# Performance work log

Hardware: AMD Instinct MI355X
Metric: run time of the kernel (lower is better)

The kernel has to match this reference:

```python
import jax, jax.numpy as jnp
import numpy as np

N_SHIFT = 23          # self.n in the torch module
OUTPUT_BIT = 8
INT31_MAX = 2147483647.0  # 2**31 - 1


def floor_ste(x):
    # straight-through floor: forward floor, backward identity
    return x + jax.lax.stop_gradient(jnp.floor(x) - x)


def int_exp_shift(x_int, scaling_factor):
    # integer-only exp approximation via shift decomposition
    x_int = x_int + floor_ste(x_int / 2.0) - floor_ste(x_int / 16.0)  # x*(1+1/2-1/16) ~ x*ln2^-1 trick
    x0_int = jax.lax.stop_gradient(jnp.floor(-1.0 / scaling_factor))   # -ln2 in integer domain (no grad)
    x_int = jnp.maximum(x_int, N_SHIFT * x0_int)
    q = floor_ste(x_int / x0_int)                 # integer quotient, in [0, N_SHIFT]
    r = x_int - x0_int * q                        # remainder
    exp_int = r / 2.0 - x0_int
    exp_int = jnp.maximum(floor_ste(exp_int * jnp.exp2(N_SHIFT - q)), 0.0)
    return exp_int


def setup_inputs() -> dict:
    key = jax.random.key(0)
    k1, _ = jax.random.split(key)
    x = jax.random.normal(k1, (64, 197, 3072), dtype=jnp.float32)
    # realistic per-tensor activation quantization scale
    scaling_factor = jnp.ones((1,), dtype=jnp.float32) * 0.02
    return {"x": x, "scaling_factor": scaling_factor}


def reference(x, scaling_factor):
    pre_x_int = x / scaling_factor                      # [B, T, H] integer-domain input
    sf_sig = scaling_factor * 1.702                     # sigmoid(1.702*x) GELU approx scale
    x_int_max = jnp.max(pre_x_int, axis=-1, keepdims=True)   # [B, T, 1]
    x_int = pre_x_int - x_int_max                       # shift for numerical range
    exp_int = int_exp_shift(x_int, sf_sig)              # exp(x - m)
    exp_int_max = int_exp_shift(-x_int_max, sf_sig)     # exp(-m) == exp(0 - m)
    exp_int_sum = jnp.minimum(exp_int + exp_int_max, INT31_MAX)
    factor = floor_ste(INT31_MAX / exp_int_sum)
    sigmoid_int = floor_ste(exp_int * factor / 2.0 ** (31 - OUTPUT_BIT + 1))
    out_sf = scaling_factor * (1.0 / 2.0 ** (OUTPUT_BIT - 1))
    x_int_out = pre_x_int * sigmoid_int
    return x_int_out * out_sf, out_sf
```

## Files before the change

kernel.cpp:

```cpp
#include <hip/hip_runtime.h>
#include <math.h>


#define ROWLEN   3072
#define NTHREADS 256

typedef float f32x4 __attribute__((ext_vector_type(4)));

__device__ __forceinline__ float int_exp_exact(float xi, float x0) {
    #pragma clang fp contract(off)
    float t = (xi + floorf(xi * 0.5f)) - floorf(xi * 0.0625f);
    t = fmaxf(t, 23.0f * x0);
    float q = floorf(t / x0);
    float r = t - x0 * q;
    float e = r * 0.5f - x0;
    e = floorf(ldexpf(e, 23 - (int)q));
    return fmaxf(e, 0.0f);
}

__device__ __forceinline__ float int_exp_fast(float xi, float x0, float inv_x0,
                                              float c23x0) {
    #pragma clang fp contract(off)
    float t = (xi + floorf(xi * 0.5f)) - floorf(xi * 0.0625f);
    t = fmaxf(t, c23x0);
    float q = floorf(t * inv_x0);
    float r = t - x0 * q;
    float e = r * 0.5f - x0;
    e = floorf(ldexpf(e, 23 - (int)q));
    return fmaxf(e, 0.0f);
}

__global__ __launch_bounds__(NTHREADS)
void intgelu_kernel(const float* __restrict__ x, const float* __restrict__ sfp,
                    float* __restrict__ out, long long scalar_idx) {
    #pragma clang fp contract(off)
    const int   row = blockIdx.x;
    const int   tid = threadIdx.x;
    const float* xr   = x   + (size_t)row * ROWLEN;
    float*       outr = out + (size_t)row * ROWLEN;

    float xv[12];
    float lmax = -INFINITY;
    #pragma unroll
    for (int c = 0; c < 3; ++c) {
        float4 v = reinterpret_cast<const float4*>(xr)[c * NTHREADS + tid];
        xv[c*4+0] = v.x; xv[c*4+1] = v.y; xv[c*4+2] = v.z; xv[c*4+3] = v.w;
        lmax = fmaxf(lmax, fmaxf(fmaxf(v.x, v.y), fmaxf(v.z, v.w)));
    }

    #pragma unroll
    for (int off = 32; off > 0; off >>= 1)
        lmax = fmaxf(lmax, __shfl_xor(lmax, off, 64));
    __shared__ float smax[NTHREADS / 64];
    if ((tid & 63) == 0) smax[tid >> 6] = lmax;
    __syncthreads();
    const float mraw = fmaxf(fmaxf(smax[0], smax[1]), fmaxf(smax[2], smax[3]));

    const float sf     = sfp[0];
    const float m      = mraw / sf;
    const float x0     = floorf(-1.0f / (sf * 1.702f));
    const float inv_x0 = 1.0f / x0;
    const float c23x0  = 23.0f * x0;
    const float em     = int_exp_exact(0.0f - m, x0);
    const float out_sf = sf * 0.0078125f;

    #pragma unroll
    for (int c = 0; c < 3; ++c) {
        f32x4 o;
        #pragma unroll
        for (int j = 0; j < 4; ++j) {
            float p  = xv[c*4+j] / sf;
            float e  = int_exp_fast(p - m, x0, inv_x0, c23x0);
            float s  = fminf(e + em, 2147483647.0f);
            float f  = floorf(2147483647.0f / s);
            float sg = floorf((e * f) * 5.9604644775390625e-8f);
            o[j] = (p * sg) * out_sf;
        }
        __builtin_nontemporal_store(o, &reinterpret_cast<f32x4*>(outr)[c * NTHREADS + tid]);
    }

    if (row == 0 && tid == 0) out[scalar_idx] = out_sf;
}

extern "C" void kernel_launch(void* const* d_in, const int* in_sizes, int n_in,
                              void* d_out, int out_size, void* d_ws, size_t ws_size,
                              hipStream_t stream) {
    const float* x   = (const float*)d_in[0];
    const float* sfp = (const float*)d_in[1];
    float*       out = (float*)d_out;
    const int nrows  = in_sizes[0] / ROWLEN;
    const long long scalar_idx = (long long)out_size - 1;
    intgelu_kernel<<<nrows, NTHREADS, 0, stream>>>(x, sfp, out, scalar_idx);
}
```

Before: 269.6 us.

## Use persistent grid-stride blocks with next-row prefetch and reciprocal-based division

Switches from one block per row to a fixed grid of 2048 persistent blocks that loop over rows. Each block prefetches the next row into registers while it reduces and computes the current one, with double-buffered shared memory so one barrier per row is enough. Full IEEE divisions are replaced by a reciprocal multiply plus an FMA correction step, and the min clamp and divide constant are adjusted. The aim is to hide load latency and cut divide cost, at the risk of fewer resident blocks, more register pressure, and small numerical differences.

Result: slower. 276.4 us (+2.5%).

```diff
diff --git a/kernel.cpp b/kernel.cpp
--- a/kernel.cpp
+++ b/kernel.cpp
@@ -4,82 +4,123 @@
 
 #define ROWLEN   3072
 #define NTHREADS 256
+#define GRIDSZ   2048
 
 typedef float f32x4 __attribute__((ext_vector_type(4)));
 
-__device__ __forceinline__ float int_exp_exact(float xi, float x0) {
+__device__ __forceinline__ float crdiv(float a, float b, float y) {
+    #pragma clang fp contract(off)
+    float q0 = a * y;
+    float r  = fmaf(-q0, b, a);
+    return fmaf(r, y, q0);
+}
+
+__device__ __forceinline__ float int_exp_fast(float xi, float x0, float y_x0,
+                                              float c23x0) {
     #pragma clang fp contract(off)
     float t = (xi + floorf(xi * 0.5f)) - floorf(xi * 0.0625f);
-    t = fmaxf(t, 23.0f * x0);
-    float q = floorf(t / x0);
+    t = fmaxf(t, c23x0);
+    float q = floorf(t * y_x0);
     float r = t - x0 * q;
     float e = r * 0.5f - x0;
     e = floorf(ldexpf(e, 23 - (int)q));
     return fmaxf(e, 0.0f);
 }
 
-__device__ __forceinline__ float int_exp_fast(float xi, float x0, float inv_x0,
-                                              float c23x0) {
+__device__ __forceinline__ float int_exp_cr(float xi, float x0, float y_x0,
+                                            float c23x0) {
     #pragma clang fp contract(off)
     float t = (xi + floorf(xi * 0.5f)) - floorf(xi * 0.0625f);
     t = fmaxf(t, c23x0);
-    float q = floorf(t * inv_x0);
+    float q = floorf(crdiv(t, x0, y_x0));
     float r = t - x0 * q;
     float e = r * 0.5f - x0;
     e = floorf(ldexpf(e, 23 - (int)q));
     return fmaxf(e, 0.0f);
 }
 
-__global__ __launch_bounds__(NTHREADS)
+__global__ __launch_bounds__(NTHREADS, 8)
 void intgelu_kernel(const float* __restrict__ x, const float* __restrict__ sfp,
-                    float* __restrict__ out, long long scalar_idx) {
+                    float* __restrict__ out, int nrows, long long scalar_idx) {
     #pragma clang fp contract(off)
-    const int   row = blockIdx.x;
-    const int   tid = threadIdx.x;
-    const float* xr   = x   + (size_t)row * ROWLEN;
-    float*       outr = out + (size_t)row * ROWLEN;
+    const int tid = threadIdx.x;
 
-    float xv[12];
-    float lmax = -INFINITY;
-    #pragma unroll
-    for (int c = 0; c < 3; ++c) {
-        float4 v = reinterpret_cast<const float4*>(xr)[c * NTHREADS + tid];
-        xv[c*4+0] = v.x; xv[c*4+1] = v.y; xv[c*4+2] = v.z; xv[c*4+3] = v.w;
-        lmax = fmaxf(lmax, fmaxf(fmaxf(v.x, v.y), fmaxf(v.z, v.w)));
+    const float sf     = sfp[0];
+    const float y_sf   = 1.0f / sf;
+    const float x0     = floorf(-1.0f / (sf * 1.702f));
+    const float y_x0   = 1.0f / x0;
+    const float c23x0  = 23.0f * x0;
+    const float out_sf = sf * 0.0078125f;
+
+    if (blockIdx.x == 0 && tid == 0) out[scalar_idx] = out_sf;
+
+    __shared__ float smax[2][NTHREADS / 64];
+
+    int row = blockIdx.x;
+    if (row >= nrows) return;
+
+    f32x4 xc[3];
+    {
+        const f32x4* xr = reinterpret_cast<const f32x4*>(x + (size_t)row * ROWLEN);
+        xc[0] = xr[0 * NTHREADS + tid];
+        xc[1] = xr[1 * NTHREADS + tid];
+        xc[2] = xr[2 * NTHREADS + tid];
     }
 
-    #pragma unroll
-    for (int off = 32; off > 0; off >>= 1)
-        lmax = fmaxf(lmax, __shfl_xor(lmax, off, 64));
-    __shared__ float smax[NTHREADS / 64];
-    if ((tid & 63) == 0) smax[tid >> 6] = lmax;
-    __syncthreads();
-    const float mraw = fmaxf(fmaxf(smax[0], smax[1]), fmaxf(smax[2], smax[3]));
+    int parity = 0;
+    for (;;) {
+        const int nextrow = row + GRIDSZ;
 
-    const float sf     = sfp[0];
-    const float m      = mraw / sf;
-    const float x0     = floorf(-1.0f / (sf * 1.702f));
-    const float inv_x0 = 1.0f / x0;
-    const float c23x0  = 23.0f * x0;
-    const float em     = int_exp_exact(0.0f - m, x0);
-    const float out_sf = sf * 0.0078125f;
+        float p[12];
+        float lmax = -INFINITY;
+        #pragma unroll
+        for (int c = 0; c < 3; ++c) {
+            #pragma unroll
+            for (int j = 0; j < 4; ++j) {
+                float xv = xc[c][j];
+                lmax = fmaxf(lmax, xv);
+                p[c * 4 + j] = crdiv(xv, sf, y_sf);
+            }
+        }
 
-    #pragma unroll
-    for (int c = 0; c < 3; ++c) {
-        f32x4 o;
+        if (nextrow < nrows) {
+            const f32x4* xn = reinterpret_cast<const f32x4*>(x + (size_t)nextrow * ROWLEN);
+            xc[0] = xn[0 * NTHREADS + tid];
+            xc[1] = xn[1 * NTHREADS + tid];
+            xc[2] = xn[2 * NTHREADS + tid];
+        }
+
         #pragma unroll
-        for (int j = 0; j < 4; ++j) {
-            float p  = xv[c*4+j] / sf;
-            float e  = int_exp_fast(p - m, x0, inv_x0, c23x0);
-            float s  = fminf(e + em, 2147483647.0f);
-            float f  = floorf(2147483647.0f / s);
-            float sg = floorf((e * f) * 5.9604644775390625e-8f);
-            o[j] = (p * sg) * out_sf;
+        for (int off = 32; off > 0; off >>= 1)
+            lmax = fmaxf(lmax, __shfl_xor(lmax, off, 64));
+        if ((tid & 63) == 0) smax[parity][tid >> 6] = lmax;
+        __syncthreads();
+        const float mraw = fmaxf(fmaxf(smax[parity][0], smax[parity][1]),
+                                 fmaxf(smax[parity][2], smax[parity][3]));
+
+        const float m  = crdiv(mraw, sf, y_sf);
+        const float em = int_exp_cr(0.0f - m, x0, y_x0, c23x0);
+
+        float* outr = out + (size_t)row * ROWLEN;
+        #pragma unroll
+        for (int c = 0; c < 3; ++c) {
+            f32x4 o;
+            #pragma unroll
+            for (int j = 0; j < 4; ++j) {
+                float pp = p[c * 4 + j];
+                float e  = int_exp_fast(pp - m, x0, y_x0, c23x0);
+                float s  = e + em;
+                float f  = floorf(2147483648.0f / s);
+                float sg = floorf((e * f) * 5.9604644775390625e-8f);
+                o[j] = (pp * sg) * out_sf;
+            }
+            __builtin_nontemporal_store(o, &reinterpret_cast<f32x4*>(outr)[c * NTHREADS + tid]);
         }
-        __builtin_nontemporal_store(o, &reinterpret_cast<f32x4*>(outr)[c * NTHREADS + tid]);
+
+        if (nextrow >= nrows) break;
+        row = nextrow;
+        parity ^= 1;
     }
-
-    if (row == 0 && tid == 0) out[scalar_idx] = out_sf;
 }
 
 extern "C" void kernel_launch(void* const* d_in, const int* in_sizes, int n_in,
@@ -90,5 +131,6 @@
     float*       out = (float*)d_out;
     const int nrows  = in_sizes[0] / ROWLEN;
     const long long scalar_idx = (long long)out_size - 1;
-    intgelu_kernel<<<nrows, NTHREADS, 0, stream>>>(x, sfp, out, scalar_idx);
+    const int grid = (nrows < GRIDSZ) ? nrows : GRIDSZ;
+    intgelu_kernel<<<grid, NTHREADS, 0, stream>>>(x, sfp, out, nrows, scalar_idx);
 }
```
